# Optimization experiments

Hardware: AMD Instinct MI355X
Metric: run time of the kernel (lower is better)

Reference implementation:

```python
import jax, jax.numpy as jnp
import numpy as np

TAU = 0.5
EPS = 1e-8
NEG = -1e30  # masked logit value (finite to keep grads clean)

B, L1, L2 = 8, 2048, 2048


def setup_inputs() -> dict:
    key = jax.random.key(0)
    k1, k2 = jax.random.split(key)
    sim_matrix = jax.random.normal(k1, (B, L1, L2), dtype=jnp.float32)
    # per-sample valid lengths in [1024, 2048] so masking is exercised but no row is empty
    lengths = jax.random.randint(k2, (B, 2), 1024, 2049, dtype=jnp.int32)
    return {"sim_matrix": sim_matrix, "lengths": lengths}


def reference(sim_matrix, lengths):
    # mask[b,i,j] = (i < lengths[b,0]) & (j < lengths[b,1])
    i_idx = jnp.arange(sim_matrix.shape[1])[None, :, None]
    j_idx = jnp.arange(sim_matrix.shape[2])[None, None, :]
    mask = (i_idx < lengths[:, 0, None, None]) & (j_idx < lengths[:, 1, None, None])

    logits = jnp.where(mask, sim_matrix / TAU, NEG)
    row_sm = jax.nn.softmax(logits, axis=-1)   # competition over L2 per row
    col_sm = jax.nn.softmax(logits, axis=-2)   # competition over L1 per column

    # geometric mean of the two assignments; zero outside valid region
    out = jnp.where(mask, jnp.sqrt(EPS + row_sm * col_sm), 0.0)
    return out
```

## Files before the change

kernel.cpp:

```cpp
#include <hip/hip_runtime.h>
#include <math.h>

#define L 2048
#define BATCH 8
#define NSPLIT 32
#define ROWS_PER_SPLIT (L / NSPLIT)
#define SENT -1e30f
#define EPSF 1e-8f

__device__ __forceinline__ void onl_upd(float& m, float& s, float x) {
    if (x > m) { s = s * __expf(m - x) + 1.0f; m = x; }
    else       { s += __expf(x - m); }
}

__device__ __forceinline__ void onl_merge(float& m, float& s, float m2, float s2) {
    float M = fmaxf(m, m2);
    s = s * __expf(m - M) + s2 * __expf(m2 - M);
    m = M;
}

__global__ __launch_bounds__(256) void row_stats_k(
    const float* __restrict__ sim, const int* __restrict__ lengths,
    float* __restrict__ rmax, float* __restrict__ rinv) {
  const int row = blockIdx.x;
  const int b = row >> 11;
  const int len1 = lengths[2 * b + 1];
  const float* p = sim + (size_t)row * L;
  const int tid = threadIdx.x;
  float m = SENT, s = 0.0f;
#pragma unroll
  for (int ph = 0; ph < 2; ++ph) {
    const int j = ph * 1024 + tid * 4;
    float4 v = *reinterpret_cast<const float4*>(p + j);
    if (j + 3 < len1) {
      onl_upd(m, s, v.x * 2.0f); onl_upd(m, s, v.y * 2.0f);
      onl_upd(m, s, v.z * 2.0f); onl_upd(m, s, v.w * 2.0f);
    } else {
      if (j + 0 < len1) onl_upd(m, s, v.x * 2.0f);
      if (j + 1 < len1) onl_upd(m, s, v.y * 2.0f);
      if (j + 2 < len1) onl_upd(m, s, v.z * 2.0f);
      if (j + 3 < len1) onl_upd(m, s, v.w * 2.0f);
    }
  }
#pragma unroll
  for (int off = 32; off > 0; off >>= 1) {
    float m2 = __shfl_xor(m, off, 64);
    float s2 = __shfl_xor(s, off, 64);
    onl_merge(m, s, m2, s2);
  }
  __shared__ float smx[4], ssm[4];
  const int wave = tid >> 6, lane = tid & 63;
  if (lane == 0) { smx[wave] = m; ssm[wave] = s; }
  __syncthreads();
  if (tid == 0) {
#pragma unroll
    for (int w = 1; w < 4; ++w) onl_merge(m, s, smx[w], ssm[w]);
    rmax[row] = m;
    rinv[row] = 1.0f / s;
  }
}

__global__ __launch_bounds__(256) void col_partial_k(
    const float* __restrict__ sim, const int* __restrict__ lengths,
    float* __restrict__ pmax, float* __restrict__ psum) {
  const int b = blockIdx.z;
  const int len0 = lengths[2 * b];
  const int j = (blockIdx.x << 10) + threadIdx.x * 4;
  const int i0 = blockIdx.y * ROWS_PER_SPLIT;
  const int iend = min(i0 + ROWS_PER_SPLIT, len0);
  float4 m = make_float4(SENT, SENT, SENT, SENT);
  float4 s = make_float4(0.f, 0.f, 0.f, 0.f);
  const float* p = sim + ((size_t)b * L + i0) * L + j;
  for (int i = i0; i < iend; ++i, p += L) {
    float4 v = *reinterpret_cast<const float4*>(p);
    onl_upd(m.x, s.x, v.x * 2.0f);
    onl_upd(m.y, s.y, v.y * 2.0f);
    onl_upd(m.z, s.z, v.z * 2.0f);
    onl_upd(m.w, s.w, v.w * 2.0f);
  }
  const size_t o = (size_t)(b * NSPLIT + blockIdx.y) * L + j;
  *reinterpret_cast<float4*>(pmax + o) = m;
  *reinterpret_cast<float4*>(psum + o) = s;
}

__global__ __launch_bounds__(256) void col_merge_k(
    const float* __restrict__ pmax, const float* __restrict__ psum,
    float* __restrict__ cmax, float* __restrict__ cinv) {
  const int idx = blockIdx.x * 256 + threadIdx.x;
  const int b = idx >> 11, j = idx & (L - 1);
  float m = SENT, s = 0.0f;
#pragma unroll 4
  for (int c = 0; c < NSPLIT; ++c) {
    const size_t o = (size_t)(b * NSPLIT + c) * L + j;
    onl_merge(m, s, pmax[o], psum[o]);
  }
  cmax[idx] = m;
  cinv[idx] = 1.0f / s;
}

__global__ __launch_bounds__(256) void finalize_k(
    const float* __restrict__ sim, const int* __restrict__ lengths,
    const float* __restrict__ rmax, const float* __restrict__ rinv,
    const float* __restrict__ cmax, const float* __restrict__ cinv,
    float* __restrict__ out) {
  const int row = blockIdx.y;
  const int b = row >> 11, i = row & (L - 1);
  const int len0 = lengths[2 * b], len1 = lengths[2 * b + 1];
  const int j = (blockIdx.x << 10) + threadIdx.x * 4;
  const size_t off = (size_t)row * L + j;
  float4 o;
  if (i >= len0) {
    o = make_float4(0.f, 0.f, 0.f, 0.f);
  } else {
    const float rm = rmax[row], ri = rinv[row];
    float4 v = *reinterpret_cast<const float4*>(sim + off);
    const size_t co = (size_t)b * L + j;
    float4 cm = *reinterpret_cast<const float4*>(cmax + co);
    float4 ci = *reinterpret_cast<const float4*>(cinv + co);
    o.x = (j + 0 < len1) ? sqrtf(EPSF + __expf(4.0f * v.x - rm - cm.x) * ri * ci.x) : 0.0f;
    o.y = (j + 1 < len1) ? sqrtf(EPSF + __expf(4.0f * v.y - rm - cm.y) * ri * ci.y) : 0.0f;
    o.z = (j + 2 < len1) ? sqrtf(EPSF + __expf(4.0f * v.z - rm - cm.z) * ri * ci.z) : 0.0f;
    o.w = (j + 3 < len1) ? sqrtf(EPSF + __expf(4.0f * v.w - rm - cm.w) * ri * ci.w) : 0.0f;
  }
  *reinterpret_cast<float4*>(out + off) = o;
}

extern "C" void kernel_launch(void* const* d_in, const int* in_sizes, int n_in,
                              void* d_out, int out_size, void* d_ws, size_t ws_size,
                              hipStream_t stream) {
  const float* sim = (const float*)d_in[0];
  const int* lengths = (const int*)d_in[1];
  float* out = (float*)d_out;
  float* ws = (float*)d_ws;

  const int NR = BATCH * L;
  float* rmax = ws;
  float* rinv = ws + NR;
  float* cmax = ws + 2 * (size_t)NR;
  float* cinv = ws + 3 * (size_t)NR;
  float* pmax = ws + 4 * (size_t)NR;
  float* psum = pmax + (size_t)BATCH * NSPLIT * L;

  hipLaunchKernelGGL(row_stats_k, dim3(NR), dim3(256), 0, stream,
                     sim, lengths, rmax, rinv);
  hipLaunchKernelGGL(col_partial_k, dim3(2, NSPLIT, BATCH), dim3(256), 0, stream,
                     sim, lengths, pmax, psum);
  hipLaunchKernelGGL(col_merge_k, dim3(NR / 256), dim3(256), 0, stream,
                     pmax, psum, cmax, cinv);
  hipLaunchKernelGGL(finalize_k, dim3(2, NR), dim3(256), 0, stream,
                     sim, lengths, rmax, rinv, cmax, cinv, out);
}
```

Baseline: 280.1 us.

## Fuse row and column softmax stats into one pass without max subtraction

Result: faster. 244.7 us (-12.6%).

```diff
diff --git a/kernel.cpp b/kernel.cpp
--- a/kernel.cpp
+++ b/kernel.cpp
@@ -3,105 +3,80 @@
 
 #define L 2048
 #define BATCH 8
-#define NSPLIT 32
-#define ROWS_PER_SPLIT (L / NSPLIT)
-#define SENT -1e30f
+#define RPS 32
+#define NSPLIT (L / RPS)
 #define EPSF 1e-8f
+#define C2 2.885390081777927f
+#define C4 5.770780163555854f
 
-__device__ __forceinline__ void onl_upd(float& m, float& s, float x) {
-    if (x > m) { s = s * __expf(m - x) + 1.0f; m = x; }
-    else       { s += __expf(x - m); }
+__device__ __forceinline__ float fexp2(float x) {
+  return __builtin_amdgcn_exp2f(x);
 }
 
-__device__ __forceinline__ void onl_merge(float& m, float& s, float m2, float s2) {
-    float M = fmaxf(m, m2);
-    s = s * __expf(m - M) + s2 * __expf(m2 - M);
-    m = M;
-}
+__global__ __launch_bounds__(512) void stats_k(
+    const float* __restrict__ sim, const int* __restrict__ lengths,
+    float* __restrict__ rinv, float* __restrict__ pcol) {
+  const int b = blockIdx.y;
+  const int islab = blockIdx.x;
+  const int len0 = lengths[2 * b], len1 = lengths[2 * b + 1];
+  const int tid = threadIdx.x;
+  const int j = tid * 4;
+  const int i0 = islab * RPS;
+  const int iend = min(i0 + RPS, len0);
 
-__global__ __launch_bounds__(256) void row_stats_k(
-    const float* __restrict__ sim, const int* __restrict__ lengths,
-    float* __restrict__ rmax, float* __restrict__ rinv) {
-  const int row = blockIdx.x;
-  const int b = row >> 11;
-  const int len1 = lengths[2 * b + 1];
-  const float* p = sim + (size_t)row * L;
-  const int tid = threadIdx.x;
-  float m = SENT, s = 0.0f;
-#pragma unroll
-  for (int ph = 0; ph < 2; ++ph) {
-    const int j = ph * 1024 + tid * 4;
-    float4 v = *reinterpret_cast<const float4*>(p + j);
-    if (j + 3 < len1) {
-      onl_upd(m, s, v.x * 2.0f); onl_upd(m, s, v.y * 2.0f);
-      onl_upd(m, s, v.z * 2.0f); onl_upd(m, s, v.w * 2.0f);
-    } else {
-      if (j + 0 < len1) onl_upd(m, s, v.x * 2.0f);
-      if (j + 1 < len1) onl_upd(m, s, v.y * 2.0f);
-      if (j + 2 < len1) onl_upd(m, s, v.z * 2.0f);
-      if (j + 3 < len1) onl_upd(m, s, v.w * 2.0f);
-    }
-  }
-#pragma unroll
-  for (int off = 32; off > 0; off >>= 1) {
-    float m2 = __shfl_xor(m, off, 64);
-    float s2 = __shfl_xor(s, off, 64);
-    onl_merge(m, s, m2, s2);
-  }
-  __shared__ float smx[4], ssm[4];
+  float4 msk;
+  msk.x = (j + 0 < len1) ? 1.f : 0.f;
+  msk.y = (j + 1 < len1) ? 1.f : 0.f;
+  msk.z = (j + 2 < len1) ? 1.f : 0.f;
+  msk.w = (j + 3 < len1) ? 1.f : 0.f;
+
+  float4 cacc = make_float4(0.f, 0.f, 0.f, 0.f);
+  __shared__ float rowpart[RPS][8];
   const int wave = tid >> 6, lane = tid & 63;
-  if (lane == 0) { smx[wave] = m; ssm[wave] = s; }
-  __syncthreads();
-  if (tid == 0) {
-#pragma unroll
-    for (int w = 1; w < 4; ++w) onl_merge(m, s, smx[w], ssm[w]);
-    rmax[row] = m;
-    rinv[row] = 1.0f / s;
-  }
-}
 
-__global__ __launch_bounds__(256) void col_partial_k(
-    const float* __restrict__ sim, const int* __restrict__ lengths,
-    float* __restrict__ pmax, float* __restrict__ psum) {
-  const int b = blockIdx.z;
-  const int len0 = lengths[2 * b];
-  const int j = (blockIdx.x << 10) + threadIdx.x * 4;
-  const int i0 = blockIdx.y * ROWS_PER_SPLIT;
-  const int iend = min(i0 + ROWS_PER_SPLIT, len0);
-  float4 m = make_float4(SENT, SENT, SENT, SENT);
-  float4 s = make_float4(0.f, 0.f, 0.f, 0.f);
   const float* p = sim + ((size_t)b * L + i0) * L + j;
   for (int i = i0; i < iend; ++i, p += L) {
     float4 v = *reinterpret_cast<const float4*>(p);
-    onl_upd(m.x, s.x, v.x * 2.0f);
-    onl_upd(m.y, s.y, v.y * 2.0f);
-    onl_upd(m.z, s.z, v.z * 2.0f);
-    onl_upd(m.w, s.w, v.w * 2.0f);
+    float4 e;
+    e.x = fexp2(v.x * C2) * msk.x;
+    e.y = fexp2(v.y * C2) * msk.y;
+    e.z = fexp2(v.z * C2) * msk.z;
+    e.w = fexp2(v.w * C2) * msk.w;
+    cacc.x += e.x; cacc.y += e.y; cacc.z += e.z; cacc.w += e.w;
+    float r = (e.x + e.y) + (e.z + e.w);
+#pragma unroll
+    for (int off = 1; off < 64; off <<= 1) r += __shfl_xor(r, off, 64);
+    if (lane == 0) rowpart[i - i0][wave] = r;
   }
-  const size_t o = (size_t)(b * NSPLIT + blockIdx.y) * L + j;
-  *reinterpret_cast<float4*>(pmax + o) = m;
-  *reinterpret_cast<float4*>(psum + o) = s;
+  __syncthreads();
+
+  if (tid < RPS) {
+    const int i = i0 + tid;
+    if (i < len0) {
+      float s = 0.f;
+#pragma unroll
+      for (int w = 0; w < 8; ++w) s += rowpart[tid][w];
+      rinv[b * L + i] = 1.0f / s;
+    }
+  }
+  const size_t o = (size_t)(b * NSPLIT + islab) * L + j;
+  *reinterpret_cast<float4*>(pcol + o) = cacc;
 }
 
 __global__ __launch_bounds__(256) void col_merge_k(
-    const float* __restrict__ pmax, const float* __restrict__ psum,
-    float* __restrict__ cmax, float* __restrict__ cinv) {
+    const float* __restrict__ pcol, float* __restrict__ cinv) {
   const int idx = blockIdx.x * 256 + threadIdx.x;
   const int b = idx >> 11, j = idx & (L - 1);
-  float m = SENT, s = 0.0f;
-#pragma unroll 4
-  for (int c = 0; c < NSPLIT; ++c) {
-    const size_t o = (size_t)(b * NSPLIT + c) * L + j;
-    onl_merge(m, s, pmax[o], psum[o]);
-  }
-  cmax[idx] = m;
+  const float* p = pcol + (size_t)b * NSPLIT * L + j;
+  float s = 0.f;
+#pragma unroll 8
+  for (int c = 0; c < NSPLIT; ++c) s += p[(size_t)c * L];
   cinv[idx] = 1.0f / s;
 }
 
 __global__ __launch_bounds__(256) void finalize_k(
     const float* __restrict__ sim, const int* __restrict__ lengths,
-    const float* __restrict__ rmax, const float* __restrict__ rinv,
-    const float* __restrict__ cmax, const float* __restrict__ cinv,
+    const float* __restrict__ rinv, const float* __restrict__ cinv,
     float* __restrict__ out) {
   const int row = blockIdx.y;
   const int b = row >> 11, i = row & (L - 1);
@@ -112,15 +87,13 @@
   if (i >= len0) {
     o = make_float4(0.f, 0.f, 0.f, 0.f);
   } else {
-    const float rm = rmax[row], ri = rinv[row];
+    const float ri = rinv[row];
     float4 v = *reinterpret_cast<const float4*>(sim + off);
-    const size_t co = (size_t)b * L + j;
-    float4 cm = *reinterpret_cast<const float4*>(cmax + co);
-    float4 ci = *reinterpret_cast<const float4*>(cinv + co);
-    o.x = (j + 0 < len1) ? sqrtf(EPSF + __expf(4.0f * v.x - rm - cm.x) * ri * ci.x) : 0.0f;
-    o.y = (j + 1 < len1) ? sqrtf(EPSF + __expf(4.0f * v.y - rm - cm.y) * ri * ci.y) : 0.0f;
-    o.z = (j + 2 < len1) ? sqrtf(EPSF + __expf(4.0f * v.z - rm - cm.z) * ri * ci.z) : 0.0f;
-    o.w = (j + 3 < len1) ? sqrtf(EPSF + __expf(4.0f * v.w - rm - cm.w) * ri * ci.w) : 0.0f;
+    float4 ci = *reinterpret_cast<const float4*>(cinv + (size_t)b * L + j);
+    o.x = (j + 0 < len1) ? sqrtf(EPSF + fexp2(v.x * C4) * ri * ci.x) : 0.f;
+    o.y = (j + 1 < len1) ? sqrtf(EPSF + fexp2(v.y * C4) * ri * ci.y) : 0.f;
+    o.z = (j + 2 < len1) ? sqrtf(EPSF + fexp2(v.z * C4) * ri * ci.z) : 0.f;
+    o.w = (j + 3 < len1) ? sqrtf(EPSF + fexp2(v.w * C4) * ri * ci.w) : 0.f;
   }
   *reinterpret_cast<float4*>(out + off) = o;
 }
@@ -134,19 +107,14 @@
   float* ws = (float*)d_ws;
 
   const int NR = BATCH * L;
-  float* rmax = ws;
-  float* rinv = ws + NR;
-  float* cmax = ws + 2 * (size_t)NR;
-  float* cinv = ws + 3 * (size_t)NR;
-  float* pmax = ws + 4 * (size_t)NR;
-  float* psum = pmax + (size_t)BATCH * NSPLIT * L;
+  float* rinv = ws;
+  float* cinv = ws + NR;
+  float* pcol = ws + 2 * (size_t)NR;
 
-  hipLaunchKernelGGL(row_stats_k, dim3(NR), dim3(256), 0, stream,
-                     sim, lengths, rmax, rinv);
-  hipLaunchKernelGGL(col_partial_k, dim3(2, NSPLIT, BATCH), dim3(256), 0, stream,
-                     sim, lengths, pmax, psum);
+  hipLaunchKernelGGL(stats_k, dim3(NSPLIT, BATCH), dim3(512), 0, stream,
+                     sim, lengths, rinv, pcol);
   hipLaunchKernelGGL(col_merge_k, dim3(NR / 256), dim3(256), 0, stream,
-                     pmax, psum, cmax, cinv);
+                     pcol, cinv);
   hipLaunchKernelGGL(finalize_k, dim3(2, NR), dim3(256), 0, stream,
-                     sim, lengths, rmax, rinv, cmax, cinv, out);
+                     sim, lengths, rinv, cinv, out);
 }
```
